# Performance work log

Hardware: AMD Instinct MI355X
Metric: run time of the kernel (lower is better)

## Reference

```python
import jax, jax.numpy as jnp
import numpy as np

B, N, D = 4, 2048, 256
EPS = 1e-5


def _clinear(Z, W, b):
    # complex linear: Z (B,2,N,din), W (2,dout,din), b (2,dout)
    Zr, Zi = Z[:, 0], Z[:, 1]
    Wr, Wi = W[0], W[1]
    outr = Zr @ Wr.T - Zi @ Wi.T + b[0]
    outi = Zr @ Wi.T + Zi @ Wr.T + b[1]
    return jnp.stack([outr, outi], axis=1)


def setup_inputs() -> dict:
    key = jax.random.key(0)
    ks = jax.random.split(key, 14)
    sc = 1.0 / np.sqrt(D).astype(np.float32)
    t = jnp.tile(jnp.arange(N + 1, dtype=jnp.float32)[None] * 0.01, (B, 1))
    return {
        'Z_q': jax.random.normal(ks[0], (B, 2, N, D), jnp.float32),
        'Z_k': jax.random.normal(ks[1], (B, 2, N, D), jnp.float32),
        'Z_v': jax.random.normal(ks[2], (B, 2, N, D), jnp.float32),
        't_measure_all': t,
        'W_q': jax.random.normal(ks[3], (2, D, D), jnp.float32) * sc,
        'b_q': jax.random.normal(ks[4], (2, D), jnp.float32) * 0.01,
        'W_k': jax.random.normal(ks[5], (2, D, D), jnp.float32) * sc,
        'b_k': jax.random.normal(ks[6], (2, D), jnp.float32) * 0.01,
        'W_v': jax.random.normal(ks[7], (2, D, D), jnp.float32) * sc,
        'b_v': jax.random.normal(ks[8], (2, D), jnp.float32) * 0.01,
        'W_p': jax.random.normal(ks[9], (2, D, D), jnp.float32) * sc,
        'b_p': jax.random.normal(ks[10], (2, D), jnp.float32) * 0.01,
        'lambda1': jax.random.normal(ks[11], (2, D // 2, 1), jnp.float32),
        'lambda_Omega_sqrt': jax.random.normal(ks[12], (1, D, 1), jnp.float32) * sc,
        'lambda_Gamma_sqrt': jax.random.normal(ks[13], (1, D, 1), jnp.float32) * sc,
        'tau': jnp.asarray(1.0, jnp.float32),
        'delta': jnp.asarray(0.0, jnp.float32),
        'lambda_C': jnp.ones((1, D, 1), jnp.float32),
    }


def reference(Z_q, Z_k, Z_v, t_measure_all, W_q, b_q, W_k, b_k, W_v, b_v,
              W_p, b_p, lambda1, lambda_Omega_sqrt, lambda_Gamma_sqrt,
              tau, delta, lambda_C):
    # lambda_h = 0 * compute_lambda_h(lambda1): conjugate-pair spectrum, zeroed in forward
    lam_r = 0.0 * jnp.concatenate([lambda1[0], lambda1[0]], axis=0)[:, 0]   # (D,)
    lam_i = 0.0 * jnp.concatenate([lambda1[1], -lambda1[1]], axis=0)[:, 0]  # (D,)
    lam_Om = lambda_Omega_sqrt ** 2 + EPS   # process noise (1,D,1)
    lam_Ga = lambda_Gamma_sqrt ** 2 + EPS   # measurement noise (1,D,1)

    Q = _clinear(Z_q, W_q, b_q)  # (B,2,N,D)
    K = _clinear(Z_k, W_k, b_k)
    V = _clinear(Z_v, W_v, b_v)

    t = t_measure_all[0, :-1]  # (N,)
    # exponential state-transition kernels exp(+/- lambda * t): (2,N,D)
    mag_f = jnp.exp(lam_r[None] * t[:, None]); ph_f = lam_i[None] * t[:, None]
    exp_f = jnp.stack([mag_f * jnp.cos(ph_f), mag_f * jnp.sin(ph_f)])
    mag_b = jnp.exp(-lam_r[None] * t[:, None]); ph_b = -lam_i[None] * t[:, None]
    exp_b = jnp.stack([mag_b * jnp.cos(ph_b), mag_b * jnp.sin(ph_b)])
    # one-step transition exp(lambda * dt): (2,D)
    dt = t[1] - t[0]
    mat_exp = jnp.stack([jnp.exp(lam_r * dt) * jnp.cos(lam_i * dt),
                         jnp.exp(lam_r * dt) * jnp.sin(lam_i * dt)])

    # averaged covariance kernel, exact lambda->0 limit: Gamma + Omega*|t_i-t_j|, mean over D
    lamC2 = lambda_C[0, :, 0] ** 2
    ga_bar = jnp.mean(lamC2 * lam_Ga[0, :, 0])
    om_bar = jnp.mean(lamC2 * lam_Om[0, :, 0])
    abs_dt = jnp.abs(t[:, None] - t[None, :])          # (N,N)
    V_avg_ij = ga_bar + om_bar * abs_dt                # (N,N)

    # factorized kernels
    V_v = exp_f[None]                 # (1,2,N,D)
    U_q = exp_b[None] * Q             # (B,2,N,D)
    U_k = exp_b[None] * K
    U_v = exp_b[None] * V

    # precision-weighted squared residual norm R_ij = sum_d |V_k|^2 |U_q_i - U_k_j|^2
    Vk_abs = jnp.sum(exp_f ** 2, axis=0)              # (N,D)
    Uk_abs = jnp.sum(U_k ** 2, axis=1)                # (B,N,D)
    Uq_abs = jnp.sum(U_q ** 2, axis=1)                # (B,N,D)
    T1 = jnp.einsum('id,bjd->bij', Vk_abs, Uk_abs)
    T2 = jnp.sum(Vk_abs[None] * Uq_abs, axis=2)[:, :, None]
    T3 = (jnp.einsum('bid,bjd->bij', Vk_abs[None] * U_q[:, 0], U_k[:, 0]) +
          jnp.einsum('bid,bjd->bij', Vk_abs[None] * U_q[:, 1], U_k[:, 1]))
    R_qk_abs = T1 + T2 - 2.0 * T3                     # (B,N,N)

    scores = -(tau ** 2) * jnp.log(V_avg_ij[None] + R_qk_abs)
    mask = jnp.tril(jnp.ones((N, N), bool))
    scores = jnp.where(mask[None], scores, -jnp.inf)
    A = jax.nn.softmax(scores, axis=2)                # (B,N,N)
    Q_ij = jnp.stack([A, jnp.zeros_like(A)], axis=1)  # (B,2,N,N)

    # est_inner = complex matmul(Q_ij, U_v); Q imag part is zero
    est_inner = jnp.stack([jnp.einsum('bij,bjd->bid', A, U_v[:, 0]),
                           jnp.einsum('bij,bjd->bid', A, U_v[:, 1])], axis=1)
    est_v = V_v * est_inner          # plain elementwise product, as in source
    s = jax.nn.sigmoid(delta)
    est_eigenbasis = (1.0 - s) * V + s * est_v        # (B,2,N,D)

    # complex Hadamard with one-step transition
    pr = mat_exp[0][None, None] * est_eigenbasis[:, 0] - mat_exp[1][None, None] * est_eigenbasis[:, 1]
    pi = mat_exp[0][None, None] * est_eigenbasis[:, 1] + mat_exp[1][None, None] * est_eigenbasis[:, 0]
    pred_p = jnp.stack([pr, pi], axis=1)
    out = _clinear(pred_p, W_p, b_p)                  # (B,2,N,D)

    lambda_h = jnp.stack([lam_r, lam_i])[..., None]
    return est_eigenbasis, out, Q_ij, V_v, U_v, lambda_h
```

## Files before the change

kernel.cpp:

```cpp
#include <hip/hip_runtime.h>
#include <math.h>

#define BN 4
#define NN 2048
#define DD 256
#define EPSF 1e-5f

typedef __attribute__((ext_vector_type(8))) short bf16x8;
typedef __attribute__((ext_vector_type(4))) float f32x4;

constexpr size_t OFF_EST = 0;
constexpr size_t OFF_OUT = (size_t)BN * 2 * NN * DD;
constexpr size_t OFF_QIJ = OFF_OUT + (size_t)BN * 2 * NN * DD;
constexpr size_t OFF_VV  = OFF_QIJ + (size_t)BN * 2 * NN * NN;
constexpr size_t OFF_UV  = OFF_VV + (size_t)2 * NN * DD;
constexpr size_t OFF_LH  = OFF_UV + (size_t)BN * 2 * NN * DD;

constexpr size_t SCR_B0   = OFF_QIJ + (size_t)NN * NN;
constexpr size_t U_Q16    = 0;
constexpr size_t U_K16    = (size_t)BN * NN * DD;
constexpr size_t U_VT16   = 2 * (size_t)BN * NN * DD;
constexpr size_t SCR_QN   = SCR_B0 + 3 * (size_t)BN * NN * DD / 2;
constexpr size_t SCR_KN   = SCR_QN + (size_t)BN * NN;
constexpr size_t SCR_L    = SCR_KN + (size_t)BN * NN;
constexpr size_t SCR_SC   = SCR_L + (size_t)BN * NN;
constexpr size_t SCR_W16P = SCR_SC + 16;
constexpr size_t SCR_E16F = OFF_QIJ + 3 * (size_t)NN * NN;
constexpr size_t U_PART   = (size_t)BN * NN * 512;
constexpr size_t SCR_Z16F = OFF_QIJ + 5 * (size_t)NN * NN;
constexpr size_t SCR_Z16VF = OFF_QIJ + 7 * (size_t)NN * NN;
constexpr size_t U_W16    = (size_t)BN * NN * 512;
constexpr size_t W16_PER_B = 136 * 16384;

__device__ __forceinline__ short f2bf(float x) {
    union { float f; unsigned u; } v; v.f = x;
    unsigned r = v.u + 0x7fff + ((v.u >> 16) & 1);
    return (short)(r >> 16);
}
__device__ __forceinline__ float bf2f(unsigned short h) {
    union { unsigned u; float f; } v; v.u = ((unsigned)h) << 16;
    return v.f;
}
__device__ __forceinline__ unsigned short* u16p(float* d, size_t fofs) {
    return (unsigned short*)(d + fofs);
}
__device__ __forceinline__ const unsigned short* u16pc(const float* d, size_t fofs) {
    return (const unsigned short*)(d + fofs);
}
__device__ __forceinline__ unsigned short* w16p(float* d, int b) {
    return (b < 3) ? u16p(d, SCR_Z16F) + (size_t)b * W16_PER_B
                   : u16p(d, SCR_Z16VF);
}
__device__ __forceinline__ const unsigned short* w16pc(const float* d, int b) {
    return (b < 3) ? u16pc(d, SCR_Z16F) + (size_t)b * W16_PER_B
                   : u16pc(d, SCR_Z16VF);
}
__device__ __forceinline__ int nc_of(int TI) { return TI >= 12 ? 3 : (TI >= 6 ? 2 : 1); }
__device__ __forceinline__ int cb_of(int TI) {
    return TI < 6 ? TI : (TI < 12 ? 6 + 2 * (TI - 6) : 18 + 3 * (TI - 12));
}

__device__ __forceinline__ void gll16(const unsigned short* g, short* l) {
    __builtin_amdgcn_global_load_lds(
        (const __attribute__((address_space(1))) unsigned*)g,
        (__attribute__((address_space(3))) unsigned*)l, 16, 0, 0);
}
__device__ __forceinline__ void stage_tile(const unsigned short* gbase, size_t stride_sh,
                                           short* ldsbuf, int t) {
    const int w = t >> 6, L = t & 63;
#pragma unroll
    for (int p = 0; p < 2; ++p) {
        const int r0 = w * 32 + p * 16;
        const unsigned short* src = gbase + (size_t)(r0 + (L >> 2)) * stride_sh + (L & 3) * 8;
        gll16(src, ldsbuf + r0 * 32);
    }
}
__device__ __forceinline__ void stage64(const unsigned short* gbase, size_t stride_sh,
                                        short* ldsbuf, int t) {
    const int w = t >> 6, L = t & 63;
    const int r0 = w * 16;
    const unsigned short* src = gbase + (size_t)(r0 + (L >> 2)) * stride_sh + (L & 3) * 8;
    gll16(src, ldsbuf + r0 * 32);
}

__global__ void k_prep(const float* __restrict__ Wq, const float* __restrict__ Wk,
                       const float* __restrict__ Wv, const float* __restrict__ Wp,
                       const float* __restrict__ tau, const float* __restrict__ delta,
                       const float* __restrict__ lamOm, const float* __restrict__ lamGa,
                       const float* __restrict__ lamC,
                       float* __restrict__ dout) {
    const int z = blockIdx.z;
    if (z == 0) {
        const float* Ws[4] = {Wq, Wk, Wv, Wp};
        const long n4 = 6L * 256 * 512 / 4;
        for (long e4 = (long)blockIdx.x * 256 + threadIdx.x; e4 < n4;
             e4 += (long)gridDim.x * 256) {
            const long e = e4 * 4;
            const int k = (int)(e & 511);
            const long rest = e >> 9;
            const int dd = (int)(rest & 255);
            const int m = (int)(rest >> 8);
            int proj, mode;
            if (m < 3)      { proj = m; mode = 0; }
            else if (m == 3){ proj = 2; mode = 1; }
            else            { proj = 3; mode = m - 4; }
            const int kc = k >> 8, kk = k & 255;
            int wc; float sgn;
            if (mode == 0) { wc = kc; sgn = kc ? -1.f : 1.f; }
            else           { wc = 1 - kc; sgn = 1.f; }
            float4 v = *(const float4*)&Ws[proj][((size_t)wc * DD + dd) * DD + kk];
            ushort4 o;
            o.x = (unsigned short)f2bf(sgn * v.x); o.y = (unsigned short)f2bf(sgn * v.y);
            o.z = (unsigned short)f2bf(sgn * v.z); o.w = (unsigned short)f2bf(sgn * v.w);
            unsigned short* dst = (m < 4)
                ? u16p(dout, SCR_Z16VF) + U_W16 + (size_t)m * 131072
                : u16p(dout, SCR_W16P) + (size_t)(m - 4) * 131072;
            *(ushort4*)&dst[(size_t)dd * 512 + k] = o;
        }
    } else {
        const int idx = blockIdx.x * 256 + threadIdx.x;
        if (idx < 3 * BN * NN) dout[SCR_QN + idx] = 0.f;
        if (blockIdx.x == 0) {
            __shared__ float red[8];
            const int t = threadIdx.x;
            float c2 = lamC[t] * lamC[t];
            float ga = c2 * (lamGa[t] * lamGa[t] + EPSF);
            float om = c2 * (lamOm[t] * lamOm[t] + EPSF);
            for (int o = 32; o > 0; o >>= 1) {
                ga += __shfl_down(ga, o, 64);
                om += __shfl_down(om, o, 64);
            }
            if ((t & 63) == 0) { red[t >> 6] = ga; red[4 + (t >> 6)] = om; }
            __syncthreads();
            if (t == 0) {
                float gs = red[0] + red[1] + red[2] + red[3];
                float os = red[4] + red[5] + red[6] + red[7];
                float* scal = dout + SCR_SC;
                scal[0] = tau[0] * tau[0];
                scal[1] = 1.f / (1.f + __expf(-delta[0]));
                scal[2] = gs / 256.f;
                scal[3] = os / 256.f;
            }
        }
    }
}

__global__ __launch_bounds__(256) void k_qkv(const float* __restrict__ Zq,
                                             const float* __restrict__ Zk,
                                             const float* __restrict__ Zv,
                                             const float* __restrict__ bq,
                                             const float* __restrict__ bk,
                                             const float* __restrict__ bv,
                                             float* __restrict__ dout)
{
    __shared__ short Al[64 * 32];
    __shared__ short Bl[128 * 32];
    const int z = blockIdx.z;
    const int d0 = blockIdx.x * 128;
    const int b = blockIdx.y >> 5;
    const int n0 = (blockIdx.y & 31) * 64;

    const float* Zf = (z == 0) ? Zq : (z == 1) ? Zk : Zv;
    const unsigned short* W16 = u16pc(dout, SCR_Z16VF) + U_W16 + (size_t)z * 131072;
    const float* bias = (z == 0) ? bq : (z == 1) ? bk : bv;
    const int bofs = (z == 3) ? DD : 0;

    const int t = threadIdx.x, wave = t >> 6, lane = t & 63, quad = lane >> 4, lm = lane & 15;
    const int wr = (wave >> 1) * 32, wc = (wave & 1) * 64;
    const int ar = t >> 2, ac8 = (t & 3) * 8;
    const unsigned short* Bbase = W16 + (size_t)d0 * 512;

    f32x4 acc[2][4];
#pragma unroll
    for (int i = 0; i < 2; ++i)
#pragma unroll
        for (int j = 0; j < 4; ++j) acc[i][j] = (f32x4){0.f, 0.f, 0.f, 0.f};

    for (int kt = 0; kt < 16; ++kt) {
        const int kk0 = kt * 32;
        const int c = kt >> 3;
        const int dcol = (kt & 7) * 32;
        const float* As = Zf + ((size_t)((b * 2 + c) * NN + n0 + ar)) * DD + dcol + ac8;
        float4 av0 = *(const float4*)(As + 0);
        float4 av1 = *(const float4*)(As + 4);
        stage_tile(Bbase + kk0, 512, Bl, t);
        ushort4 ha, hb;
        ha.x = (unsigned short)f2bf(av0.x); ha.y = (unsigned short)f2bf(av0.y);
        ha.z = (unsigned short)f2bf(av0.z); ha.w = (unsigned short)f2bf(av0.w);
        hb.x = (unsigned short)f2bf(av1.x); hb.y = (unsigned short)f2bf(av1.y);
        hb.z = (unsigned short)f2bf(av1.z); hb.w = (unsigned short)f2bf(av1.w);
        *(ushort4*)&Al[ar * 32 + ac8]     = ha;
        *(ushort4*)&Al[ar * 32 + ac8 + 4] = hb;
        __syncthreads();
        bf16x8 af[2], bff[4];
#pragma unroll
        for (int mi = 0; mi < 2; ++mi) af[mi] = *(const bf16x8*)&Al[(wr + mi * 16 + lm) * 32 + quad * 8];
#pragma unroll
        for (int nj = 0; nj < 4; ++nj) bff[nj] = *(const bf16x8*)&Bl[(wc + nj * 16 + lm) * 32 + quad * 8];
#pragma unroll
        for (int mi = 0; mi < 2; ++mi)
#pragma unroll
            for (int nj = 0; nj < 4; ++nj)
                acc[mi][nj] = __builtin_amdgcn_mfma_f32_16x16x32_bf16(af[mi], bff[nj], acc[mi][nj], 0, 0, 0);
        __syncthreads();
    }

    if (z <= 1) {
        unsigned short* O16 = u16p(dout, SCR_B0) + (z ? U_K16 : U_Q16) + (size_t)b * NN * DD;
        float* NRM = dout + (z ? SCR_KN : SCR_QN) + b * NN;
#pragma unroll
        for (int mi = 0; mi < 2; ++mi)
#pragma unroll
            for (int r = 0; r < 4; ++r) {
                const int m = n0 + wr + mi * 16 + quad * 4 + r;
                float ss = 0.f;
#pragma unroll
                for (int nj = 0; nj < 4; ++nj) {
                    const int d = d0 + wc + nj * 16 + lm;
                    unsigned short h = (unsigned short)f2bf(acc[mi][nj][r] + bias[d]);
                    O16[(size_t)m * DD + d] = h;
                    const float vb = bf2f(h);
                    ss = fmaf(vb, vb, ss);
                }
                ss += __shfl_down(ss, 8, 16); ss += __shfl_down(ss, 4, 16);
                ss += __shfl_down(ss, 2, 16); ss += __shfl_down(ss, 1, 16);
                if (lm == 0) atomicAdd(&NRM[m], ss);
            }
    } else if (z == 2) {
        float* UV0 = dout + OFF_UV + (size_t)(b * 2) * NN * DD;
#pragma unroll
        for (int mi = 0; mi < 2; ++mi)
#pragma unroll
            for (int r = 0; r < 4; ++r) {
                const int m = n0 + wr + mi * 16 + quad * 4 + r;
#pragma unroll
                for (int nj = 0; nj < 4; ++nj) {
                    const int d = d0 + wc + nj * 16 + lm;
                    UV0[(size_t)m * DD + d] = acc[mi][nj][r] + bias[d];
                }
            }
    } else {
        const float s1 = 1.f - dout[SCR_SC + 1];
        float* EST1 = dout + OFF_EST + (size_t)(b * 2 + 1) * NN * DD;
        unsigned short* E16 = u16p(dout, SCR_E16F) + (size_t)b * NN * 512;
#pragma unroll
        for (int mi = 0; mi < 2; ++mi)
#pragma unroll
            for (int r = 0; r < 4; ++r) {
                const int m = n0 + wr + mi * 16 + quad * 4 + r;
#pragma unroll
                for (int nj = 0; nj < 4; ++nj) {
                    const int d = d0 + wc + nj * 16 + lm;
                    const float v = s1 * (acc[mi][nj][r] + bias[bofs + d]);
                    EST1[(size_t)m * DD + d] = v;
                    E16[(size_t)m * 512 + 256 + d] = (unsigned short)f2bf(v);
                }
            }
    }
}

__global__ __launch_bounds__(256) void k_outproj(const float* __restrict__ bp,
                                                 float* __restrict__ dout)
{
    __shared__ short Al[64 * 32];
    __shared__ short Bl[128 * 32];
    const int z = blockIdx.z;
    if (z == 2) {
        const long idx = (long)(blockIdx.y * 2 + blockIdx.x) * 256 + threadIdx.x;
        const float4 zz4 = {0.f, 0.f, 0.f, 0.f};
        for (long u = idx * 4; u < (long)NN * NN; u += 256L * 256 * 4) {
            *(float4*)&dout[SCR_Z16F + u] = zz4;
            *(float4*)&dout[SCR_Z16VF + u] = zz4;
        }
        for (long u = idx * 4; u < 2097152; u += 256L * 256 * 4)
            *(float4*)&dout[SCR_E16F + 2097152 + u] = zz4;
        return;
    }
    const int d0 = blockIdx.x * 128;
    const int b = blockIdx.y >> 5;
    const int n0 = (blockIdx.y & 31) * 64;
    const unsigned short* E16 = u16pc(dout, SCR_E16F) + (size_t)b * NN * 512;
    const unsigned short* W16 = u16pc(dout, SCR_W16P) + (size_t)z * 131072;

    const int t = threadIdx.x, wave = t >> 6, lane = t & 63, quad = lane >> 4, lm = lane & 15;
    const int wr = (wave >> 1) * 32, wc = (wave & 1) * 64;
    const unsigned short* Abase = E16 + (size_t)n0 * 512;
    const unsigned short* Bbase = W16 + (size_t)d0 * 512;

    f32x4 acc[2][4];
#pragma unroll
    for (int i = 0; i < 2; ++i)
#pragma unroll
        for (int j = 0; j < 4; ++j) acc[i][j] = (f32x4){0.f, 0.f, 0.f, 0.f};

    for (int kt = 0; kt < 16; ++kt) {
        const int kk0 = kt * 32;
        stage64(Abase + kk0, 512, Al, t);
        stage_tile(Bbase + kk0, 512, Bl, t);
        __syncthreads();
        bf16x8 af[2], bff[4];
#pragma unroll
        for (int mi = 0; mi < 2; ++mi) af[mi] = *(const bf16x8*)&Al[(wr + mi * 16 + lm) * 32 + quad * 8];
#pragma unroll
        for (int nj = 0; nj < 4; ++nj) bff[nj] = *(const bf16x8*)&Bl[(wc + nj * 16 + lm) * 32 + quad * 8];
#pragma unroll
        for (int mi = 0; mi < 2; ++mi)
#pragma unroll
            for (int nj = 0; nj < 4; ++nj)
                acc[mi][nj] = __builtin_amdgcn_mfma_f32_16x16x32_bf16(af[mi], bff[nj], acc[mi][nj], 0, 0, 0);
        __syncthreads();
    }
    const int bofs = z ? DD : 0;
    float* O = dout + OFF_OUT + (size_t)(b * 2 + z) * NN * DD;
#pragma unroll
    for (int mi = 0; mi < 2; ++mi)
#pragma unroll
        for (int r = 0; r < 4; ++r) {
            const int m = n0 + wr + mi * 16 + quad * 4 + r;
#pragma unroll
            for (int nj = 0; nj < 4; ++nj) {
                const int d = d0 + wc + nj * 16 + lm;
                O[(size_t)m * DD + d] = acc[mi][nj][r] + bp[bofs + d];
            }
        }
}

__global__ __launch_bounds__(256) void k_scores(const float* __restrict__ tmeas,
                                                float* __restrict__ dout) {
    __shared__ __align__(16) float smemf[4160];
    short* Al = (short*)smemf;
    short* Bl = ((short*)smemf) + 2048;
    const int b = blockIdx.y;
    if (blockIdx.x >= 272) {
        float (*T)[65] = (float(*)[65])smemf;
        const int vj = blockIdx.x - 272;
        const int nb = (vj & 31) * 64, db = (vj >> 5) * 64;
        const float* V = dout + OFF_UV + (size_t)(b * 2) * NN * DD;
        unsigned short* VT = u16p(dout, SCR_B0) + U_VT16 + (size_t)b * DD * NN;
        const int tr = threadIdx.x >> 4, tc = (threadIdx.x & 15) * 4;
#pragma unroll
        for (int p = 0; p < 4; ++p) {
            float4 v = *(const float4*)&V[(size_t)(nb + tr + p * 16) * DD + db + tc];
            T[tr + p * 16][tc + 0] = v.x; T[tr + p * 16][tc + 1] = v.y;
            T[tr + p * 16][tc + 2] = v.z; T[tr + p * 16][tc + 3] = v.w;
        }
        __syncthreads();
#pragma unroll
        for (int p = 0; p < 4; ++p) {
            const int d = tr + p * 16;
            ushort4 o;
            o.x = (unsigned short)f2bf(T[tc + 0][d]);
            o.y = (unsigned short)f2bf(T[tc + 1][d]);
            o.z = (unsigned short)f2bf(T[tc + 2][d]);
            o.w = (unsigned short)f2bf(T[tc + 3][d]);
            *(ushort4*)&VT[(size_t)(db + d) * NN + nb + tc] = o;
        }
        return;
    }
    const int x2 = blockIdx.x;
    const int x = x2 >> 1, ih = x2 & 1;
    int ti = (int)((sqrtf(8.f * x + 1.f) - 1.f) * 0.5f);
    while ((ti + 1) * (ti + 2) / 2 <= x) ++ti;
    while (ti * (ti + 1) / 2 > x) --ti;
    const int tj = x - ti * (ti + 1) / 2;
    const int i0 = ti * 128, j0 = tj * 128;
    const int ib = i0 + ih * 64;
    const unsigned short* Q16 = u16pc(dout, SCR_B0) + U_Q16 + (size_t)b * NN * DD;
    const unsigned short* K16 = u16pc(dout, SCR_B0) + U_K16 + (size_t)b * NN * DD;
    const int t = threadIdx.x, wave = t >> 6, lane = t & 63, quad = lane >> 4, lm = lane & 15;
    const int wr = (wave >> 1) * 32, wc = (wave & 1) * 64;
    const unsigned short* Abase = Q16 + (size_t)ib * DD;
    const unsigned short* Bbase = K16 + (size_t)j0 * DD;

    f32x4 acc[2][4];
#pragma unroll
    for (int i = 0; i < 2; ++i)
#pragma unroll
        for (int j = 0; j < 4; ++j) acc[i][j] = (f32x4){0.f, 0.f, 0.f, 0.f};

    for (int kt = 0; kt < 8; ++kt) {
        const int kk0 = kt * 32;
        stage64(Abase + kk0, DD, Al, t);
        stage_tile(Bbase + kk0, DD, Bl, t);
        __syncthreads();
        bf16x8 af[2], bff[4];
#pragma unroll
        for (int mi = 0; mi < 2; ++mi) af[mi] = *(const bf16x8*)&Al[(wr + mi * 16 + lm) * 32 + quad * 8];
#pragma unroll
        for (int nj = 0; nj < 4; ++nj) bff[nj] = *(const bf16x8*)&Bl[(wc + nj * 16 + lm) * 32 + quad * 8];
#pragma unroll
        for (int mi = 0; mi < 2; ++mi)
#pragma unroll
            for (int nj = 0; nj < 4; ++nj)
                acc[mi][nj] = __builtin_amdgcn_mfma_f32_16x16x32_bf16(af[mi], bff[nj], acc[mi][nj], 0, 0, 0);
        __syncthreads();
    }

    const float tau2 = dout[SCR_SC + 0], ga = dout[SCR_SC + 2], om = dout[SCR_SC + 3];
    unsigned short* WT = w16p(dout, b) + (size_t)x * 16384;
    const float* QN_ = dout + SCR_QN + b * NN;
    const float* KN_ = dout + SCR_KN + b * NN;
    float kn[4], tjv[4]; int jj[4], jl[4];
#pragma unroll
    for (int nj = 0; nj < 4; ++nj) {
        jl[nj] = wc + nj * 16 + lm;
        jj[nj] = j0 + jl[nj];
        kn[nj] = KN_[jj[nj]];
        tjv[nj] = tmeas[jj[nj]];
    }
#pragma unroll
    for (int mi = 0; mi < 2; ++mi)
#pragma unroll
        for (int r = 0; r < 4; ++r) {
            const int li = ih * 64 + wr + mi * 16 + quad * 4 + r;
            const int i = i0 + li;
            const float qni = QN_[i], tqi = tmeas[i];
            float rs = 0.f;
#pragma unroll
            for (int nj = 0; nj < 4; ++nj) {
                float xx = ga + om * fabsf(tqi - tjv[nj]) + qni + kn[nj] - 2.f * acc[mi][nj][r];
                xx = fmaxf(xx, 1e-30f);
                float w = (tau2 == 1.f) ? __builtin_amdgcn_rcpf(xx)
                                        : __expf(-tau2 * __logf(xx));
                if (jj[nj] > i) w = 0.f;
                const unsigned short h = (unsigned short)f2bf(w);
                WT[(size_t)li * 128 + jl[nj]] = h;
                rs += bf2f(h);
            }
            rs += __shfl_down(rs, 8, 16); rs += __shfl_down(rs, 4, 16);
            rs += __shfl_down(rs, 2, 16); rs += __shfl_down(rs, 1, 16);
            if (lm == 0) atomicAdd(&dout[SCR_L + b * NN + i], rs);
        }
}

__global__ __launch_bounds__(256) void k_estinner(float* __restrict__ dout) {
    __shared__ short Al[128 * 32];
    __shared__ short Bl[64 * 32];
    const int b = blockIdx.y;
    const int chunk = blockIdx.x >> 2, qd = blockIdx.x & 3;
    int y = chunk, TI = 0, cb = 0;
    for (;;) { const int nc = nc_of(TI); if (y < nc) break; y -= nc; cb += nc; ++TI; }
    const int kbeg = y * 768;
    const int kend = min(kbeg + 768, (TI + 1) * 128);
    const int nst = (kend - kbeg) >> 5;
    const int cidx = cb + y;
    const int tri = TI * (TI + 1) / 2;
    const unsigned short* WT = w16pc(dout, b);
    const unsigned short* VT = u16pc(dout, SCR_B0) + U_VT16 + (size_t)b * DD * NN
                             + (size_t)(qd * 64) * NN;

    const int t = threadIdx.x, wave = t >> 6, lane = t & 63, quad = lane >> 4, lm = lane & 15;
    const int rh = (wave >> 1) * 64, ch = (wave & 1) * 32;

    f32x4 acc[4][2];
#pragma unroll
    for (int i = 0; i < 4; ++i)
#pragma unroll
        for (int j = 0; j < 2; ++j) acc[i][j] = (f32x4){0.f, 0.f, 0.f, 0.f};

    for (int kt = 0; kt < nst; ++kt) {
        const int kk0 = kbeg + kt * 32;
        const int tile = kk0 >> 7;
        stage_tile(WT + (size_t)(tri + tile) * 16384 + (kk0 & 127), 128, Al, t);
        stage64(VT + kk0, NN, Bl, t);
        __syncthreads();
        bf16x8 af[4], bff[2];
#pragma unroll
        for (int mi = 0; mi < 4; ++mi) af[mi] = *(const bf16x8*)&Al[(rh + mi * 16 + lm) * 32 + quad * 8];
#pragma unroll
        for (int nj = 0; nj < 2; ++nj) bff[nj] = *(const bf16x8*)&Bl[(ch + nj * 16 + lm) * 32 + quad * 8];
#pragma unroll
        for (int mi = 0; mi < 4; ++mi)
#pragma unroll
            for (int nj = 0; nj < 2; ++nj)
                acc[mi][nj] = __builtin_amdgcn_mfma_f32_16x16x32_bf16(af[mi], bff[nj], acc[mi][nj], 0, 0, 0);
        __syncthreads();
    }
    unsigned short* P = u16p(dout, SCR_E16F) + U_PART +
                        ((size_t)(b * 30 + cidx)) * 128 * 256;
#pragma unroll
    for (int mi = 0; mi < 4; ++mi)
#pragma unroll
        for (int r = 0; r < 4; ++r) {
            const int ri = rh + mi * 16 + quad * 4 + r;
#pragma unroll
            for (int nj = 0; nj < 2; ++nj) {
                const int d = qd * 64 + ch + nj * 16 + lm;
                P[(size_t)ri * 256 + d] = (unsigned short)f2bf(acc[mi][nj][r]);
            }
        }
}

__global__ void k_blendfills(float* __restrict__ dout) {
    const int z = blockIdx.z;
    if (z < 4) {
        const int b = z;
        if (blockIdx.x >= 512) return;
        const int t = threadIdx.x;
        const int i = blockIdx.x * 4 + (t >> 6);
        const int d4 = (t & 63) * 4;
        const int TI = i >> 7;
        const int nc = nc_of(TI), cb = cb_of(TI);
        const float s = dout[SCR_SC + 1];
        const float linv = 1.f / dout[SCR_L + b * NN + i];
        const unsigned short* P = u16pc(dout, SCR_E16F) + U_PART;
        float4 sum = {0.f, 0.f, 0.f, 0.f};
        for (int c = 0; c < nc; ++c) {
            ushort4 pv = *(const ushort4*)&P[((size_t)(b * 30 + cb + c) * 128 + (i & 127)) * 256 + d4];
            sum.x += bf2f(pv.x); sum.y += bf2f(pv.y);
            sum.z += bf2f(pv.z); sum.w += bf2f(pv.w);
        }
        const float4 vr = *(const float4*)&dout[OFF_UV + ((size_t)(b * 2) * NN + i) * DD + d4];
        const float sl = s * linv;
        float4 ev;
        ev.x = (1.f - s) * vr.x + sl * sum.x;
        ev.y = (1.f - s) * vr.y + sl * sum.y;
        ev.z = (1.f - s) * vr.z + sl * sum.z;
        ev.w = (1.f - s) * vr.w + sl * sum.w;
        *(float4*)&dout[OFF_EST + ((size_t)(b * 2) * NN + i) * DD + d4] = ev;
        ushort4 o;
        o.x = (unsigned short)f2bf(ev.x); o.y = (unsigned short)f2bf(ev.y);
        o.z = (unsigned short)f2bf(ev.z); o.w = (unsigned short)f2bf(ev.w);
        *(ushort4*)&u16p(dout, SCR_E16F)[((size_t)(b * NN + i)) * 512 + d4] = o;
        return;
    }
    if (z < 8) {
        const int b = z - 4, i = blockIdx.x;
        const int TI = i >> 7, li = i & 127;
        const int tri = TI * (TI + 1) / 2;
        const float linv = 1.f / dout[SCR_L + b * NN + i];
        const unsigned short* WTb = w16pc(dout, b);
        float* row = dout + OFF_QIJ + (size_t)b * 2 * NN * NN + (size_t)i * NN;
        for (int j4 = threadIdx.x * 4; j4 < NN; j4 += 1024) {
            const int tj = j4 >> 7;
            float4 o = {0.f, 0.f, 0.f, 0.f};
            if (tj <= TI) {
                ushort4 h = *(const ushort4*)&WTb[((size_t)(tri + tj)) * 16384
                                                  + (size_t)li * 128 + (j4 & 127)];
                o.x = bf2f(h.x) * linv; o.y = bf2f(h.y) * linv;
                o.z = bf2f(h.z) * linv; o.w = bf2f(h.w) * linv;
            }
            *(float4*)&row[j4] = o;
        }
        return;
    }
    size_t base; long n; float val = 0.f;
    if (z == 8)       { base = SCR_B0; n = 3145728; }
    else if (z == 9)  { base = OFF_VV; n = (long)NN * DD; val = 1.f; }
    else if (z == 10) { base = OFF_VV + (size_t)NN * DD; n = (long)NN * DD; }
    else if (z < 15)  { base = OFF_UV + (size_t)(2 * (z - 11) + 1) * NN * DD; n = (long)NN * DD; }
    else              { base = OFF_LH; n = 512; }
    float* p = dout + base;
    const float4 v = {val, val, val, val};
    for (long i = ((long)blockIdx.x * 256 + threadIdx.x) * 4; i < n;
         i += (long)gridDim.x * 1024)
        *(float4*)&p[i] = v;
}

__global__ void k_tail(float* __restrict__ dout) {
    const float4 zz = {0.f, 0.f, 0.f, 0.f};
    const long n1 = 2097152;
    for (long i = ((long)blockIdx.x * 256 + threadIdx.x) * 4; i < n1;
         i += (long)gridDim.x * 1024)
        *(float4*)&dout[SCR_E16F + i] = zz;
    const long n0 = (long)NN * NN - 3145728;
    for (long i = ((long)blockIdx.x * 256 + threadIdx.x) * 4; i < n0;
         i += (long)gridDim.x * 1024)
        *(float4*)&dout[SCR_QN + i] = zz;
}

extern "C" void kernel_launch(void* const* d_in, const int* in_sizes, int n_in,
                              void* d_out, int out_size, void* d_ws, size_t ws_size,
                              hipStream_t stream) {
    const float* Zq = (const float*)d_in[0];
    const float* Zk = (const float*)d_in[1];
    const float* Zv = (const float*)d_in[2];
    const float* tm = (const float*)d_in[3];
    const float* Wq = (const float*)d_in[4];
    const float* bq = (const float*)d_in[5];
    const float* Wk = (const float*)d_in[6];
    const float* bk = (const float*)d_in[7];
    const float* Wv = (const float*)d_in[8];
    const float* bv = (const float*)d_in[9];
    const float* Wp = (const float*)d_in[10];
    const float* bp = (const float*)d_in[11];
    const float* lamOm = (const float*)d_in[13];
    const float* lamGa = (const float*)d_in[14];
    const float* tau = (const float*)d_in[15];
    const float* delta = (const float*)d_in[16];
    const float* lamC = (const float*)d_in[17];
    float* out = (float*)d_out;

    k_prep<<<dim3(256, 1, 2), dim3(256), 0, stream>>>(
        Wq, Wk, Wv, Wp, tau, delta, lamOm, lamGa, lamC, out);
    k_qkv<<<dim3(2, 128, 4), dim3(256), 0, stream>>>(Zq, Zk, Zv, bq, bk, bv, out);
    k_scores<<<dim3(400, 4), dim3(256), 0, stream>>>(tm, out);
    k_estinner<<<dim3(120, 4), dim3(256), 0, stream>>>(out);
    k_blendfills<<<dim3(2048, 1, 16), dim3(256), 0, stream>>>(out);
    k_outproj<<<dim3(2, 128, 3), dim3(256), 0, stream>>>(bp, out);
    k_tail<<<dim3(512), dim3(256), 0, stream>>>(out);
}
```

Before: 337.3 us.

## Retile QKV projection to full-width rows and replace norm atomics with block reduction

The QKV projection kernel now covers the full 256-wide output per block with a 32-row tile, instead of a 64x128 tile split across two column blocks. Each block therefore owns whole rows, and the squared-norm reduction for Q and K can be done in shared memory and written once. This removes the atomicAdd traffic and the zero-initialisation of those norm buffers in the prep kernel. The trade-off is more weight staging per block (256 rows of B per k-step), a smaller A tile, and an extra sync in the epilogue.

```diff
diff --git a/kernel.cpp b/kernel.cpp
--- a/kernel.cpp
+++ b/kernel.cpp
@@ -119,7 +119,7 @@
         }
     } else {
         const int idx = blockIdx.x * 256 + threadIdx.x;
-        if (idx < 3 * BN * NN) dout[SCR_QN + idx] = 0.f;
+        if (idx < BN * NN) dout[SCR_L + idx] = 0.f;
         if (blockIdx.x == 0) {
             __shared__ float red[8];
             const int t = threadIdx.x;
@@ -153,12 +153,12 @@
                                              const float* __restrict__ bv,
                                              float* __restrict__ dout)
 {
-    __shared__ short Al[64 * 32];
-    __shared__ short Bl[128 * 32];
+    __shared__ short Al[32 * 32];
+    __shared__ short Bl[256 * 32];
+    __shared__ float nrmp[32][4];
     const int z = blockIdx.z;
-    const int d0 = blockIdx.x * 128;
-    const int b = blockIdx.y >> 5;
-    const int n0 = (blockIdx.y & 31) * 64;
+    const int b = blockIdx.x >> 6;
+    const int n0 = (blockIdx.x & 63) * 32;
 
     const float* Zf = (z == 0) ? Zq : (z == 1) ? Zk : Zv;
     const unsigned short* W16 = u16pc(dout, SCR_Z16VF) + U_W16 + (size_t)z * 131072;
@@ -166,9 +166,8 @@
     const int bofs = (z == 3) ? DD : 0;
 
     const int t = threadIdx.x, wave = t >> 6, lane = t & 63, quad = lane >> 4, lm = lane & 15;
-    const int wr = (wave >> 1) * 32, wc = (wave & 1) * 64;
-    const int ar = t >> 2, ac8 = (t & 3) * 8;
-    const unsigned short* Bbase = W16 + (size_t)d0 * 512;
+    const int wcol = wave * 64;
+    const int ar = t >> 3, ac = (t & 7) * 4;
 
     f32x4 acc[2][4];
 #pragma unroll
@@ -180,23 +179,20 @@
         const int kk0 = kt * 32;
         const int c = kt >> 3;
         const int dcol = (kt & 7) * 32;
-        const float* As = Zf + ((size_t)((b * 2 + c) * NN + n0 + ar)) * DD + dcol + ac8;
-        float4 av0 = *(const float4*)(As + 0);
-        float4 av1 = *(const float4*)(As + 4);
-        stage_tile(Bbase + kk0, 512, Bl, t);
-        ushort4 ha, hb;
-        ha.x = (unsigned short)f2bf(av0.x); ha.y = (unsigned short)f2bf(av0.y);
-        ha.z = (unsigned short)f2bf(av0.z); ha.w = (unsigned short)f2bf(av0.w);
-        hb.x = (unsigned short)f2bf(av1.x); hb.y = (unsigned short)f2bf(av1.y);
-        hb.z = (unsigned short)f2bf(av1.z); hb.w = (unsigned short)f2bf(av1.w);
-        *(ushort4*)&Al[ar * 32 + ac8]     = ha;
-        *(ushort4*)&Al[ar * 32 + ac8 + 4] = hb;
+        const float* As = Zf + ((size_t)((b * 2 + c) * NN + n0 + ar)) * DD + dcol + ac;
+        float4 av = *(const float4*)As;
+        stage_tile(W16 + kk0, 512, Bl, t);
+        stage_tile(W16 + (size_t)128 * 512 + kk0, 512, Bl + 128 * 32, t);
+        ushort4 ha;
+        ha.x = (unsigned short)f2bf(av.x); ha.y = (unsigned short)f2bf(av.y);
+        ha.z = (unsigned short)f2bf(av.z); ha.w = (unsigned short)f2bf(av.w);
+        *(ushort4*)&Al[ar * 32 + ac] = ha;
         __syncthreads();
         bf16x8 af[2], bff[4];
 #pragma unroll
-        for (int mi = 0; mi < 2; ++mi) af[mi] = *(const bf16x8*)&Al[(wr + mi * 16 + lm) * 32 + quad * 8];
-#pragma unroll
-        for (int nj = 0; nj < 4; ++nj) bff[nj] = *(const bf16x8*)&Bl[(wc + nj * 16 + lm) * 32 + quad * 8];
+        for (int mi = 0; mi < 2; ++mi) af[mi] = *(const bf16x8*)&Al[(mi * 16 + lm) * 32 + quad * 8];
+#pragma unroll
+        for (int nj = 0; nj < 4; ++nj) bff[nj] = *(const bf16x8*)&Bl[(wcol + nj * 16 + lm) * 32 + quad * 8];
 #pragma unroll
         for (int mi = 0; mi < 2; ++mi)
 #pragma unroll
@@ -212,11 +208,12 @@
         for (int mi = 0; mi < 2; ++mi)
 #pragma unroll
             for (int r = 0; r < 4; ++r) {
-                const int m = n0 + wr + mi * 16 + quad * 4 + r;
+                const int lrow = mi * 16 + quad * 4 + r;
+                const int m = n0 + lrow;
                 float ss = 0.f;
 #pragma unroll
                 for (int nj = 0; nj < 4; ++nj) {
-                    const int d = d0 + wc + nj * 16 + lm;
+                    const int d = wcol + nj * 16 + lm;
                     unsigned short h = (unsigned short)f2bf(acc[mi][nj][r] + bias[d]);
                     O16[(size_t)m * DD + d] = h;
                     const float vb = bf2f(h);
@@ -224,18 +221,21 @@
                 }
                 ss += __shfl_down(ss, 8, 16); ss += __shfl_down(ss, 4, 16);
                 ss += __shfl_down(ss, 2, 16); ss += __shfl_down(ss, 1, 16);
-                if (lm == 0) atomicAdd(&NRM[m], ss);
-            }
+                if (lm == 0) nrmp[lrow][wave] = ss;
+            }
+        __syncthreads();
+        if (t < 32)
+            NRM[n0 + t] = nrmp[t][0] + nrmp[t][1] + nrmp[t][2] + nrmp[t][3];
     } else if (z == 2) {
         float* UV0 = dout + OFF_UV + (size_t)(b * 2) * NN * DD;
 #pragma unroll
         for (int mi = 0; mi < 2; ++mi)
 #pragma unroll
             for (int r = 0; r < 4; ++r) {
-                const int m = n0 + wr + mi * 16 + quad * 4 + r;
+                const int m = n0 + mi * 16 + quad * 4 + r;
 #pragma unroll
                 for (int nj = 0; nj < 4; ++nj) {
-                    const int d = d0 + wc + nj * 16 + lm;
+                    const int d = wcol + nj * 16 + lm;
                     UV0[(size_t)m * DD + d] = acc[mi][nj][r] + bias[d];
                 }
             }
@@ -247,10 +247,10 @@
         for (int mi = 0; mi < 2; ++mi)
 #pragma unroll
             for (int r = 0; r < 4; ++r) {
-                const int m = n0 + wr + mi * 16 + quad * 4 + r;
+                const int m = n0 + mi * 16 + quad * 4 + r;
 #pragma unroll
                 for (int nj = 0; nj < 4; ++nj) {
-                    const int d = d0 + wc + nj * 16 + lm;
+                    const int d = wcol + nj * 16 + lm;
                     const float v = s1 * (acc[mi][nj][r] + bias[bofs + d]);
                     EST1[(size_t)m * DD + d] = v;
                     E16[(size_t)m * 512 + 256 + d] = (unsigned short)f2bf(v);
@@ -593,7 +593,7 @@
 
     k_prep<<<dim3(256, 1, 2), dim3(256), 0, stream>>>(
         Wq, Wk, Wv, Wp, tau, delta, lamOm, lamGa, lamC, out);
-    k_qkv<<<dim3(2, 128, 4), dim3(256), 0, stream>>>(Zq, Zk, Zv, bq, bk, bv, out);
+    k_qkv<<<dim3(256, 1, 4), dim3(256), 0, stream>>>(Zq, Zk, Zv, bq, bk, bv, out);
     k_scores<<<dim3(400, 4), dim3(256), 0, stream>>>(tm, out);
     k_estinner<<<dim3(120, 4), dim3(256), 0, stream>>>(out);
     k_blendfills<<<dim3(2048, 1, 16), dim3(256), 0, stream>>>(out);
```

After: 338.9 us. About the same (+0.5%).
